# Kernel optimization log

Measured on AMD Instinct MI355X. Metric: run time of the kernel, lower is better.

Reference implementation:

```python
import jax, jax.numpy as jnp
from jax import lax
import numpy as np

NHEADS = 8

def _conv_block2d(x, w, b):
    y = lax.conv_general_dilated(x, w, (2, 2), [(1, 1), (1, 1)],
                                 dimension_numbers=('NCHW', 'OIHW', 'NCHW'))
    return jax.nn.gelu(y + b[None, :, None, None])

def _conv_block3d(x, w, b):
    y = lax.conv_general_dilated(x, w, (2, 2, 2), [(1, 1)] * 3,
                                 dimension_numbers=('NCDHW', 'OIDHW', 'NCDHW'))
    return jax.nn.gelu(y + b[None, :, None, None, None])

def _layernorm(x, g, b, eps=1e-5):
    mu = x.mean(-1, keepdims=True)
    var = x.var(-1, keepdims=True)
    return (x - mu) / jnp.sqrt(var + eps) * g + b

def _neighborhood_attn(x, g, bln, qkv_w, qkv_b, proj_w, proj_b, dw=5, hw=7, ww=7):
    # x: [B, C, D, H, W]; 3D neighborhood attention, window (dw,hw,ww), zero-pad + mask
    B, C, D, H, W = x.shape
    h, hd = NHEADS, C // NHEADS
    xt = jnp.transpose(x, (0, 2, 3, 4, 1))               # [B,D,H,W,C]
    y = _layernorm(xt, g, bln)
    qkv = y @ qkv_w + qkv_b                               # [B,D,H,W,3C]
    qkv = qkv.reshape(B, D, H, W, 3, h, hd)
    qkv = jnp.transpose(qkv, (4, 0, 5, 6, 1, 2, 3))       # [3,B,h,hd,D,H,W]
    q, k, v = qkv[0] * (hd ** -0.5), qkv[1], qkv[2]
    pz, py, px = dw // 2, hw // 2, ww // 2
    pad = ((0, 0), (0, 0), (0, 0), (pz, pz), (py, py), (px, px))
    kp, vp = jnp.pad(k, pad), jnp.pad(v, pad)
    valid = jnp.pad(jnp.ones((D, H, W), x.dtype), ((pz, pz), (py, py), (px, px)))
    offs = jnp.stack(jnp.meshgrid(jnp.arange(dw), jnp.arange(hw), jnp.arange(ww), indexing='ij'), -1).reshape(-1, 3)

    def score_step(_, o):
        ks = lax.dynamic_slice(kp, (0, 0, 0, o[0], o[1], o[2]), (B, h, hd, D, H, W))
        m = lax.dynamic_slice(valid, (o[0], o[1], o[2]), (D, H, W))
        return None, ((q * ks).sum(2), m)

    _, (scores, masks) = lax.scan(score_step, None, offs)  # [245,B,h,D,H,W],[245,D,H,W]
    neg = jnp.finfo(scores.dtype).min
    scores = jnp.where(masks[:, None, None] > 0, scores, neg)
    probs = jax.nn.softmax(scores, axis=0)

    def out_step(acc, xs):
        o, p = xs
        vs = lax.dynamic_slice(vp, (0, 0, 0, o[0], o[1], o[2]), (B, h, hd, D, H, W))
        return acc + p[:, :, None] * vs, None

    out0 = jnp.zeros((B, h, hd, D, H, W), x.dtype)
    out, _ = lax.scan(out_step, out0, (offs, probs))
    out = jnp.transpose(out, (0, 3, 4, 5, 1, 2)).reshape(B, D, H, W, C)
    out = out @ proj_w + proj_b
    return x + jnp.transpose(out, (0, 4, 1, 2, 3))

def setup_inputs() -> dict:
    key = jax.random.key(0)
    ks = jax.random.split(key, 16)
    rn = lambda i, shp, s: jax.random.normal(ks[i], shp, jnp.float32) * s
    return {
        'x_2d': rn(0, (1, 8, 256, 512), 1.0),
        'x_3d': rn(1, (1, 5, 24, 256, 512), 1.0),
        'sw0': rn(2, (128, 8, 3, 3), 0.02), 'sb0': jnp.zeros((128,), jnp.float32),
        'sw1': rn(3, (256, 128, 3, 3), 0.02), 'sb1': jnp.zeros((256,), jnp.float32),
        'sw2': rn(4, (512, 256, 3, 3), 0.02), 'sb2': jnp.zeros((512,), jnp.float32),
        'pw0': rn(5, (128, 5, 3, 3, 3), 0.02), 'pb0': jnp.zeros((128,), jnp.float32),
        'pw1': rn(6, (256, 128, 3, 3, 3), 0.02), 'pb1': jnp.zeros((256,), jnp.float32),
        'pw2': rn(7, (512, 256, 3, 3, 3), 0.02), 'pb2': jnp.zeros((512,), jnp.float32),
        'lat_w': rn(8, (512, 512, 1, 1, 1), 0.02), 'lat_b': jnp.zeros((512,), jnp.float32),
        'ln_g': jnp.ones((3, 512), jnp.float32), 'ln_b': jnp.zeros((3, 512), jnp.float32),
        'qkv_w': rn(9, (3, 512, 1536), 0.02), 'qkv_b': jnp.zeros((3, 1536), jnp.float32),
        'proj_w': rn(10, (3, 512, 512), 0.02), 'proj_b': jnp.zeros((3, 512), jnp.float32),
    }

def reference(x_2d, x_3d, sw0, sb0, sw1, sb1, sw2, sb2,
              pw0, pb0, pw1, pb1, pw2, pb2, lat_w, lat_b,
              ln_g, ln_b, qkv_w, qkv_b, proj_w, proj_b):
    s = x_2d
    for w_, b_ in ((sw0, sb0), (sw1, sb1), (sw2, sb2)):
        s = _conv_block2d(s, w_, b_)
    p = x_3d
    for w_, b_ in ((pw0, pb0), (pw1, pb1), (pw2, pb2)):
        p = _conv_block3d(p, w_, b_)
    feats = jnp.concatenate([p, s[:, :, None]], axis=2)   # [B,512,D/8+1,H/8,W/8]
    lat = lax.conv_general_dilated(feats, lat_w, (1, 1, 1), 'VALID',
                                   dimension_numbers=('NCDHW', 'OIDHW', 'NCDHW'))
    lat = lat + lat_b[None, :, None, None, None]
    for i in range(3):
        lat = _neighborhood_attn(lat, ln_g[i], ln_b[i], qkv_w[i], qkv_b[i], proj_w[i], proj_b[i])
    return lat
```

## Files before the change

### kernel.cpp

```cpp
#include <hip/hip_runtime.h>
#include <hip/hip_bf16.h>
#include <math.h>

typedef __hip_bfloat16 bf16;
typedef __attribute__((ext_vector_type(8))) short s8v;
typedef __attribute__((ext_vector_type(4))) float f4v;

__device__ __forceinline__ float ldf(const float* p) { return *p; }
__device__ __forceinline__ float ldf(const bf16* p) { return __bfloat162float(*p); }
__device__ __forceinline__ void stf(float* p, float v) { *p = v; }
__device__ __forceinline__ void stf(bf16* p, float v) { *p = __float2bfloat16(v); }

__device__ __forceinline__ float gelu_tanh(float x) {
    float x3 = x * x * x;
    return 0.5f * x * (1.f + tanhf(0.7978845608028654f * (x + 0.044715f * x3)));
}
__device__ __forceinline__ unsigned short bfbits(float x) {
    bf16 t = __float2bfloat16(x);
    return *(unsigned short*)&t;
}

__device__ __forceinline__ void gload16(const bf16* g, bf16* l)
{
    __builtin_amdgcn_global_load_lds(
        (const __attribute__((address_space(1))) unsigned int*)g,
        (__attribute__((address_space(3))) unsigned int*)l,
        16, 0, 0);
}

__global__ __launch_bounds__(256) void fill0_k(uint4* __restrict__ p, int n16)
{
    int i = blockIdx.x * 256 + threadIdx.x;
    if (i < n16) p[i] = uint4{0u, 0u, 0u, 0u};
}

__global__ __launch_bounds__(256) void wprep_k(const float* __restrict__ w, bf16* __restrict__ wr,
                                               int OC, int IC, int T)
{
    int i = blockIdx.x * 256 + threadIdx.x;
    if (i >= OC * IC * T) return;
    int t = i % T; int rem = i / T; int ic = rem % IC; int oc = rem / IC;
    wr[((size_t)t * OC + oc) * IC + ic] = __float2bfloat16(w[i]);
}

__global__ __launch_bounds__(256) void w1prep_k(const float* __restrict__ w, bf16* __restrict__ o,
                                                int OC, int nic, int ntap, int Kp)
{
    int i = blockIdx.x * 256 + threadIdx.x;
    if (i >= OC * Kp) return;
    int oc = i / Kp, k = i - oc * Kp;
    float v = 0.f;
    if (k < nic * ntap) {
        int tap = k / nic, ic = k - tap * nic;
        v = w[((size_t)oc * nic + ic) * ntap + tap];
    }
    o[i] = __float2bfloat16(v);
}

__global__ __launch_bounds__(256) void tprep_k(const float* __restrict__ w, bf16* __restrict__ wt,
                                               int K, int N)
{
    int i = blockIdx.x * 256 + threadIdx.x;
    if (i >= K * N) return;
    int n = i % N, k = i / N;
    wt[(size_t)n * K + k] = __float2bfloat16(w[i]);
}

__global__ __launch_bounds__(256) void cast_k(const float* __restrict__ w, bf16* __restrict__ o, int n)
{
    int i = blockIdx.x * 256 + threadIdx.x;
    if (i < n) o[i] = __float2bfloat16(w[i]);
}

__global__ __launch_bounds__(256) void im2col3d_k(const float* __restrict__ x, bf16* __restrict__ A, int od0)
{
    int gid = blockIdx.x * 256 + threadIdx.x;
    int m = gid / 20, kg = gid - 20 * (gid / 20);
    int ow = m & 255, rowid = m >> 8;
    int oh = rowid & 127, od = od0 + (rowid >> 7);
    int iz0 = 2 * od - 1, iy0 = 2 * oh - 1, ix0 = 2 * ow - 1;
    union { uint4 u; unsigned short h[8]; } pk;
#pragma unroll
    for (int j = 0; j < 8; j++) {
        int k = kg * 8 + j;
        float v = 0.f;
        if (k < 135) {
            int tap = k / 5, ic = k - tap * 5;
            int kz = tap / 9, r = tap - kz * 9;
            int ky = r / 3, kx = r - ky * 3;
            int iz = iz0 + kz, iy = iy0 + ky, ix = ix0 + kx;
            if ((unsigned)iz < 24u && (unsigned)iy < 256u && (unsigned)ix < 512u)
                v = x[(((size_t)ic * 24 + iz) * 256 + iy) * 512 + ix];
        }
        pk.h[j] = bfbits(v);
    }
    *(uint4*)&A[(size_t)m * 160 + kg * 8] = pk.u;
}

__global__ __launch_bounds__(256) void im2col2d_k(const float* __restrict__ x, bf16* __restrict__ A)
{
    int gid = blockIdx.x * 256 + threadIdx.x;
    int m = gid / 12, kg = gid - 12 * (gid / 12);
    int ow = m & 255, oh = m >> 8;
    int iy0 = 2 * oh - 1, ix0 = 2 * ow - 1;
    union { uint4 u; unsigned short h[8]; } pk;
#pragma unroll
    for (int j = 0; j < 8; j++) {
        int k = kg * 8 + j;
        float v = 0.f;
        if (k < 72) {
            int tap = k >> 3, ic = k & 7;
            int ky = tap / 3, kx = tap - ky * 3;
            int iy = iy0 + ky, ix = ix0 + kx;
            if ((unsigned)iy < 256u && (unsigned)ix < 512u)
                v = x[((size_t)ic * 256 + iy) * 512 + ix];
        }
        pk.h[j] = bfbits(v);
    }
    *(uint4*)&A[(size_t)m * 96 + kg * 8] = pk.u;
}

__global__ __launch_bounds__(256) void conv1_gemm(
    const bf16* __restrict__ A, const bf16* __restrict__ W, const float* __restrict__ bias,
    bf16* __restrict__ out, int M, int Kp, int rowOff)
{
    __shared__ __align__(16) bf16 As[128 * 32];
    __shared__ __align__(16) bf16 Bs[128 * 32];
    int tid = threadIdx.x;
    int m0 = blockIdx.x * 128;
    int wave = tid >> 6, lane = tid & 63;
    int wb = tid & 192;
    int wm = (wave >> 1) * 64, wn = (wave & 1) * 64;
    int lm = lane & 15, lq = lane >> 4;
    f4v acc[4][4];
#pragma unroll
    for (int i = 0; i < 4; i++)
#pragma unroll
        for (int j = 0; j < 4; j++) acc[i][j] = f4v{0.f, 0.f, 0.f, 0.f};
    for (int k0 = 0; k0 < Kp; k0 += 32) {
        __syncthreads();
#pragma unroll
        for (int c = 0; c < 2; c++) {
            int i = c * 256 + tid;
            int row = i >> 2, kq = i & 3;
            gload16(&A[(size_t)(m0 + row) * Kp + k0 + kq * 8], &As[(c * 256 + wb) * 8]);
            gload16(&W[(size_t)row * Kp + k0 + kq * 8], &Bs[(c * 256 + wb) * 8]);
        }
        __syncthreads();
        s8v af[4], bfr[4];
#pragma unroll
        for (int mi = 0; mi < 4; mi++) af[mi] = *(const s8v*)&As[(wm + mi * 16 + lm) * 32 + lq * 8];
#pragma unroll
        for (int ni = 0; ni < 4; ni++) bfr[ni] = *(const s8v*)&Bs[(wn + ni * 16 + lm) * 32 + lq * 8];
#pragma unroll
        for (int mi = 0; mi < 4; mi++)
#pragma unroll
            for (int ni = 0; ni < 4; ni++)
                acc[mi][ni] = __builtin_amdgcn_mfma_f32_16x16x32_bf16(af[mi], bfr[ni], acc[mi][ni], 0, 0, 0);
    }
#pragma unroll
    for (int mi = 0; mi < 4; mi++)
#pragma unroll
        for (int ni = 0; ni < 4; ni++)
#pragma unroll
            for (int r = 0; r < 4; r++) {
                int m = m0 + wm + mi * 16 + lq * 4 + r;
                int n = wn + ni * 16 + lm;
                int row = rowOff + (m >> 8), x = m & 255;
                float v = acc[mi][ni][r] + bias[n];
                out[((size_t)row * 258 + 1 + x) * 128 + n] = __float2bfloat16(gelu_tanh(v));
            }
}

template <int BM, int KD>
__global__ __launch_bounds__(256) void conv_mfma2(
    const bf16* __restrict__ in, const bf16* __restrict__ wr, const float* __restrict__ bias,
    bf16* __restrict__ out, int ID, int IH, int IWp, int IC,
    int OH, int OC, int OWS, int outPad, int nx)
{
    constexpr int NI = (BM == 128) ? 4 : 2;
    __shared__ __align__(16) bf16 As[3 * BM * 32];
    __shared__ __align__(16) bf16 Bs[3 * 128 * 32];
    int tid = threadIdx.x;
    int nwg = gridDim.x;
    int bl = blockIdx.x;
    int swz = (bl & 7) * (nwg >> 3) + (bl >> 3);
    int n0 = (swz % nx) * 128;
    int rowid = swz / nx;
    int od = rowid / OH, oh = rowid % OH;
    int wave = tid >> 6, lane = tid & 63;
    int wb = tid & 192;
    int wm = (BM == 128) ? (wave >> 1) * 64 : 0;
    int wn = (BM == 128) ? (wave & 1) * 64 : wave * 32;
    int lm = lane & 15, lq = lane >> 4;
    f4v acc[4][NI];
#pragma unroll
    for (int i = 0; i < 4; i++)
#pragma unroll
        for (int j = 0; j < NI; j++) acc[i][j] = f4v{0.f, 0.f, 0.f, 0.f};

    for (int kz = 0; kz < KD; kz++) {
        int iz = (KD == 3) ? (2 * od + kz - 1) : 0;
        if ((unsigned)iz >= (unsigned)ID) continue;
        for (int ky = 0; ky < 3; ky++) {
            int iy = 2 * oh + ky - 1;
            if ((unsigned)iy >= (unsigned)IH) continue;
            const bf16* inrow = in + ((size_t)iz * IH + iy) * IWp * IC;
            const bf16* wbase = wr + (size_t)((kz * 3 + ky) * 3) * OC * IC;
            for (int kb = 0; kb < IC; kb += 32) {
                __syncthreads();
#pragma unroll
                for (int c = 0; c < (3 * BM) / 64; c++) {
                    int i = c * 256 + tid;
                    int kx = i / (BM * 4);
                    int r = i - kx * (BM * 4);
                    int m = r >> 2, sub = r & 3;
                    gload16(&inrow[(size_t)(2 * m + kx) * IC + kb + sub * 8],
                            &As[(c * 256 + wb) * 8]);
                }
#pragma unroll
                for (int c = 0; c < 6; c++) {
                    int i = c * 256 + tid;
                    int t3 = i >> 9, r = i & 511, n = r >> 2, sub = r & 3;
                    gload16(&wbase[((size_t)t3 * OC + n0 + n) * IC + kb + sub * 8],
                            &Bs[(c * 256 + wb) * 8]);
                }
                __syncthreads();
#pragma unroll
                for (int kx = 0; kx < 3; kx++) {
                    s8v af[4], bfr[NI];
#pragma unroll
                    for (int mi = 0; mi < 4; mi++)
                        af[mi] = *(const s8v*)&As[(kx * BM + wm + mi * 16 + lm) * 32 + lq * 8];
#pragma unroll
                    for (int ni = 0; ni < NI; ni++)
                        bfr[ni] = *(const s8v*)&Bs[(kx * 128 + wn + ni * 16 + lm) * 32 + lq * 8];
#pragma unroll
                    for (int mi = 0; mi < 4; mi++)
#pragma unroll
                        for (int ni = 0; ni < NI; ni++)
                            acc[mi][ni] = __builtin_amdgcn_mfma_f32_16x16x32_bf16(af[mi], bfr[ni], acc[mi][ni], 0, 0, 0);
                }
            }
        }
    }
    size_t orowbase = ((size_t)rowid * OWS + outPad) * OC;
#pragma unroll
    for (int mi = 0; mi < 4; mi++)
#pragma unroll
        for (int ni = 0; ni < NI; ni++)
#pragma unroll
            for (int r = 0; r < 4; r++) {
                int m = wm + mi * 16 + lq * 4 + r;
                int n = n0 + wn + ni * 16 + lm;
                float v = acc[mi][ni][r] + bias[n];
                out[orowbase + (size_t)m * OC + n] = __float2bfloat16(gelu_tanh(v));
            }
}

template <typename OutT, int RES, int VT>
__global__ __launch_bounds__(256) void gemm_bt(
    const bf16* __restrict__ A, const bf16* __restrict__ Bt, const float* __restrict__ bias,
    OutT* __restrict__ C, const float* __restrict__ res, bf16* __restrict__ vt,
    int M, int N, int K)
{
    __shared__ __align__(16) bf16 As[128 * 32];
    __shared__ __align__(16) bf16 Bs[128 * 32];
    int tid = threadIdx.x;
    int n0 = blockIdx.x * 128, m0 = blockIdx.y * 128;
    int wave = tid >> 6, lane = tid & 63;
    int wb = tid & 192;
    int wm = (wave >> 1) * 64, wn = (wave & 1) * 64;
    int lm = lane & 15, lq = lane >> 4;
    f4v acc[4][4];
#pragma unroll
    for (int i = 0; i < 4; i++)
#pragma unroll
        for (int j = 0; j < 4; j++) acc[i][j] = f4v{0.f, 0.f, 0.f, 0.f};
    for (int k0 = 0; k0 < K; k0 += 32) {
        __syncthreads();
#pragma unroll
        for (int c = 0; c < 2; c++) {
            int i = c * 256 + tid;
            int row = i >> 2, kq = i & 3;
            gload16(&A[(size_t)(m0 + row) * K + k0 + kq * 8], &As[(c * 256 + wb) * 8]);
            gload16(&Bt[(size_t)(n0 + row) * K + k0 + kq * 8], &Bs[(c * 256 + wb) * 8]);
        }
        __syncthreads();
        s8v af[4], bfr[4];
#pragma unroll
        for (int mi = 0; mi < 4; mi++) af[mi] = *(const s8v*)&As[(wm + mi * 16 + lm) * 32 + lq * 8];
#pragma unroll
        for (int ni = 0; ni < 4; ni++) bfr[ni] = *(const s8v*)&Bs[(wn + ni * 16 + lm) * 32 + lq * 8];
#pragma unroll
        for (int mi = 0; mi < 4; mi++)
#pragma unroll
            for (int ni = 0; ni < 4; ni++)
                acc[mi][ni] = __builtin_amdgcn_mfma_f32_16x16x32_bf16(af[mi], bfr[ni], acc[mi][ni], 0, 0, 0);
    }
#pragma unroll
    for (int mi = 0; mi < 4; mi++)
#pragma unroll
        for (int ni = 0; ni < 4; ni++) {
            int n = n0 + wn + ni * 16 + lm;
            int mbase = m0 + wm + mi * 16 + lq * 4;
            float b = bias[n];
            if (VT && n >= 1024) {
                ushort4 pk;
                pk.x = bfbits(acc[mi][ni][0] + b);
                pk.y = bfbits(acc[mi][ni][1] + b);
                pk.z = bfbits(acc[mi][ni][2] + b);
                pk.w = bfbits(acc[mi][ni][3] + b);
                *(ushort4*)&vt[(size_t)(n - 1024) * 8192 + mbase] = pk;
            }
#pragma unroll
            for (int r = 0; r < 4; r++) {
                int m = mbase + r;
                float v = acc[mi][ni][r] + b;
                if (RES) v += res[(size_t)m * N + n];
                stf(&C[(size_t)m * N + n], v);
            }
        }
}

__global__ __launch_bounds__(256) void ln_k(
    const float* __restrict__ lat, const float* __restrict__ g, const float* __restrict__ b,
    bf16* __restrict__ y)
{
    int tok = blockIdx.x * 4 + (threadIdx.x >> 6);
    int lane = threadIdx.x & 63;
    const float4* row = (const float4*)&lat[(size_t)tok * 512 + lane * 8];
    float4 a = row[0], c = row[1];
    float s = a.x + a.y + a.z + a.w + c.x + c.y + c.z + c.w;
    float ss = a.x * a.x + a.y * a.y + a.z * a.z + a.w * a.w
             + c.x * c.x + c.y * c.y + c.z * c.z + c.w * c.w;
#pragma unroll
    for (int off = 32; off; off >>= 1) {
        s += __shfl_xor(s, off);
        ss += __shfl_xor(ss, off);
    }
    float mu = s * (1.f / 512.f);
    float var = ss * (1.f / 512.f) - mu * mu;
    float rstd = rsqrtf(var + 1e-5f);
    const float4* gp = (const float4*)&g[lane * 8];
    const float4* bp = (const float4*)&b[lane * 8];
    float4 g0 = gp[0], g1 = gp[1], b0 = bp[0], b1 = bp[1];
    union { uint4 u; unsigned short h[8]; } pk;
    pk.h[0] = bfbits((a.x - mu) * rstd * g0.x + b0.x);
    pk.h[1] = bfbits((a.y - mu) * rstd * g0.y + b0.y);
    pk.h[2] = bfbits((a.z - mu) * rstd * g0.z + b0.z);
    pk.h[3] = bfbits((a.w - mu) * rstd * g0.w + b0.w);
    pk.h[4] = bfbits((c.x - mu) * rstd * g1.x + b1.x);
    pk.h[5] = bfbits((c.y - mu) * rstd * g1.y + b1.y);
    pk.h[6] = bfbits((c.z - mu) * rstd * g1.z + b1.z);
    pk.h[7] = bfbits((c.w - mu) * rstd * g1.w + b1.w);
    *(uint4*)&y[(size_t)tok * 512 + lane * 8] = pk.u;
}

__global__ __launch_bounds__(512) void natt_mfma(
    const bf16* __restrict__ qkv, const bf16* __restrict__ vT, bf16* __restrict__ o)
{
    __shared__ __align__(16) char smem[40960];
    float* mlb = (float*)smem;
    float* obuf = (float*)(smem + 8192);
    int tid = threadIdx.x;
    int bx = blockIdx.x;
    int rd = bx >> 5, rh = bx & 31;
    int d = (rd == 0) ? 1 : (rd == 1) ? 2 : (rd == 2) ? 0 : 3;
    int h = (rh < 26) ? (rh + 3) : (rh == 26) ? 2 : (rh == 27) ? 29
          : (rh == 28) ? 1 : (rh == 29) ? 30 : (rh == 30) ? 0 : 31;
    int rowid = d * 32 + h;
    int head = blockIdx.y;
    int rowbase = rowid * 64;
    int hoff = head * 64;
    int wave = tid >> 6, lane = tid & 63;
    int olane = wave & 3, rhalf = wave >> 2;
    int lm = lane & 15, lq = lane >> 4;
    char* qsb = smem;
    bf16* pb = (bf16*)(smem + 8192 + olane * 8192);

    {
        int row = tid >> 3, sub = tid & 7;
        *(uint4*)(qsb + row * 128 + ((sub * 16) ^ ((row & 7) << 4))) =
            *(const uint4*)&qkv[(size_t)(rowbase + row) * 1536 + hoff + sub * 8];
    }
    {
        uint4 z{0u, 0u, 0u, 0u};
        uint4* zp = (uint4*)(smem + 8192);
        zp[tid] = z; zp[tid + 512] = z; zp[tid + 1024] = z; zp[tid + 1536] = z;
    }
    __syncthreads();

    f4v Oa[2][4];
#pragma unroll
    for (int i = 0; i < 2; i++)
#pragma unroll
        for (int j = 0; j < 4; j++) Oa[i][j] = f4v{0.f, 0.f, 0.f, 0.f};
    float mr[2][4], lr[2][4];
#pragma unroll
    for (int i = 0; i < 2; i++)
#pragma unroll
        for (int j = 0; j < 4; j++) { mr[i][j] = -1e30f; lr[i][j] = 0.f; }

    for (int idx = olane; idx < 35; idx += 4) {
        int dz = idx / 7 - 2, dy = idx % 7 - 3;
        int zz = d + dz, yy = h + dy;
        if ((unsigned)zz >= 4u || (unsigned)yy >= 32u) continue;
        int kbase = (zz * 32 + yy) * 64;
        s8v kf[4][2];
#pragma unroll
        for (int ni = 0; ni < 4; ni++)
#pragma unroll
            for (int c = 0; c < 2; c++)
                kf[ni][c] = *(const s8v*)&qkv[(size_t)(kbase + ni * 16 + lm) * 1536 + 512 + hoff + c * 32 + lq * 8];
#pragma unroll
        for (int mj = 0; mj < 2; mj++) {
            int mi = rhalf * 2 + mj;
            int qrow = mi * 16 + lm;
            s8v qc0 = *(const s8v*)(qsb + qrow * 128 + ((lq * 16) ^ ((qrow & 7) << 4)));
            s8v qc1 = *(const s8v*)(qsb + qrow * 128 + ((64 + lq * 16) ^ ((qrow & 7) << 4)));
            f4v s[4];
#pragma unroll
            for (int ni = 0; ni < 4; ni++) s[ni] = f4v{0.f, 0.f, 0.f, 0.f};
            __builtin_amdgcn_s_setprio(1);
#pragma unroll
            for (int ni = 0; ni < 4; ni++)
                s[ni] = __builtin_amdgcn_mfma_f32_16x16x32_bf16(qc0, kf[ni][0], s[ni], 0, 0, 0);
#pragma unroll
            for (int ni = 0; ni < 4; ni++)
                s[ni] = __builtin_amdgcn_mfma_f32_16x16x32_bf16(qc1, kf[ni][1], s[ni], 0, 0, 0);
            __builtin_amdgcn_s_setprio(0);
#pragma unroll
            for (int r = 0; r < 4; r++) {
                int w0 = mi * 16 + lq * 4 + r;
                float s0v = s[0][r], s1v = s[1][r], s2v = s[2][r], s3v = s[3][r];
                int t = w0 + 8 - lm;
                int niq = (t < 0) ? 0 : (t >> 4);
                niq = (niq > 3) ? 3 : niq;
                float vlo = (niq & 1) ? s1v : s0v;
                float vhi = (niq & 1) ? s3v : s2v;
                float v = (niq & 2) ? vhi : vlo;
                int col = (niq << 4) | lm;
                int dlt = col - w0;
                float vv = ((unsigned)(dlt + 3) <= 6u) ? v * 0.125f : -1e30f;
                float rm = vv;
#pragma unroll
                for (int off = 1; off <= 8; off <<= 1)
                    rm = fmaxf(rm, __shfl_xor(rm, off));
                float mo = mr[mj][r];
                float mn = mo;
                if (__any(rm > mo)) {
                    mn = fmaxf(mo, rm);
                    float al = __expf(mo - mn);
                    mr[mj][r] = mn;
                    lr[mj][r] *= al;
#pragma unroll
                    for (int nd = 0; nd < 4; nd++)
                        Oa[mj][nd][r] *= al;
                }
                float p = __expf(vv - mn);
                float rs = p;
#pragma unroll
                for (int off = 1; off <= 8; off <<= 1)
                    rs += __shfl_xor(rs, off);
                lr[mj][r] += rs;
                pb[(w0 << 6) + (col ^ ((w0 & 7) << 3))] = __float2bfloat16(p);
            }
        }
        s8v vf[4][2];
#pragma unroll
        for (int nd = 0; nd < 4; nd++)
#pragma unroll
            for (int c = 0; c < 2; c++)
                vf[nd][c] = *(const s8v*)&vT[(size_t)(hoff + nd * 16 + lm) * 8192 + kbase + c * 32 + lq * 8];
        __asm__ __volatile__("s_waitcnt lgkmcnt(0)" ::: "memory");
        __builtin_amdgcn_sched_barrier(0);
#pragma unroll
        for (int c = 0; c < 2; c++) {
            s8v pf[2];
#pragma unroll
            for (int mj = 0; mj < 2; mj++) {
                int mi = rhalf * 2 + mj;
                pf[mj] = *(const s8v*)&pb[((mi * 16 + lm) << 6) + ((c * 32 + lq * 8) ^ ((lm & 7) << 3))];
            }
            __builtin_amdgcn_s_setprio(1);
#pragma unroll
            for (int mj = 0; mj < 2; mj++)
#pragma unroll
                for (int nd = 0; nd < 4; nd++)
                    Oa[mj][nd] = __builtin_amdgcn_mfma_f32_16x16x32_bf16(pf[mj], vf[nd][c], Oa[mj][nd], 0, 0, 0);
            __builtin_amdgcn_s_setprio(0);
        }
    }
    __syncthreads();
    if (lm == 0) {
#pragma unroll
        for (int mj = 0; mj < 2; mj++)
#pragma unroll
            for (int r = 0; r < 4; r++) {
                int row = (rhalf * 2 + mj) * 16 + lq * 4 + r;
                mlb[olane * 128 + row] = mr[mj][r];
                mlb[olane * 128 + 64 + row] = lr[mj][r];
            }
    }
    __syncthreads();
    for (int wv = 0; wv < 4; wv++) {
        if (olane == wv) {
#pragma unroll
            for (int mj = 0; mj < 2; mj++)
#pragma unroll
                for (int r = 0; r < 4; r++) {
                    int row = (rhalf * 2 + mj) * 16 + lq * 4 + r;
                    float M = fmaxf(fmaxf(mlb[row], mlb[128 + row]),
                                    fmaxf(mlb[256 + row], mlb[384 + row]));
                    float sc = __expf(mr[mj][r] - M);
#pragma unroll
                    for (int nd = 0; nd < 4; nd++) {
                        int ci = row * 65 + nd * 16 + lm;
                        float add = Oa[mj][nd][r] * sc;
                        obuf[ci] = (wv == 0) ? add : (obuf[ci] + add);
                    }
                }
        }
        __syncthreads();
    }
    {
        int row = tid >> 3, cb = (tid & 7) * 8;
        float m0 = mlb[row], m1 = mlb[128 + row], m2 = mlb[256 + row], m3 = mlb[384 + row];
        float M = fmaxf(fmaxf(m0, m1), fmaxf(m2, m3));
        float L = mlb[64 + row] * __expf(m0 - M) + mlb[192 + row] * __expf(m1 - M)
                + mlb[320 + row] * __expf(m2 - M) + mlb[448 + row] * __expf(m3 - M);
        float inv = 1.f / L;
        union { uint4 u; unsigned short hs[8]; } pk;
#pragma unroll
        for (int j = 0; j < 8; j++)
            pk.hs[j] = bfbits(obuf[row * 65 + cb + j] * inv);
        *(uint4*)&o[(size_t)(rowbase + row) * 512 + hoff + cb] = pk.u;
    }
}

__global__ __launch_bounds__(256) void tout_k(const float* __restrict__ lat, float* __restrict__ out)
{
    __shared__ float t[64][65];
    int p0 = blockIdx.x * 64, c0 = blockIdx.y * 64;
    for (int i = threadIdx.x; i < 4096; i += 256) {
        int r = i >> 6, cc = i & 63;
        t[r][cc] = lat[(size_t)(p0 + r) * 512 + c0 + cc];
    }
    __syncthreads();
    for (int i = threadIdx.x; i < 4096; i += 256) {
        int cc = i >> 6, r = i & 63;
        out[(size_t)(c0 + cc) * 8192 + p0 + r] = t[r][cc];
    }
}

extern "C" void kernel_launch(void* const* d_in, const int* in_sizes, int n_in,
                              void* d_out, int out_size, void* d_ws, size_t ws_size,
                              hipStream_t stream)
{
    const float* x2d = (const float*)d_in[0];
    const float* x3d = (const float*)d_in[1];
    const float* sw0 = (const float*)d_in[2];
    const float* sb0 = (const float*)d_in[3];
    const float* sw1 = (const float*)d_in[4];
    const float* sb1 = (const float*)d_in[5];
    const float* sw2 = (const float*)d_in[6];
    const float* sb2 = (const float*)d_in[7];
    const float* pw0 = (const float*)d_in[8];
    const float* pb0 = (const float*)d_in[9];
    const float* pw1 = (const float*)d_in[10];
    const float* pb1 = (const float*)d_in[11];
    const float* pw2 = (const float*)d_in[12];
    const float* pb2 = (const float*)d_in[13];
    const float* latw = (const float*)d_in[14];
    const float* latb = (const float*)d_in[15];
    const float* lng = (const float*)d_in[16];
    const float* lnb = (const float*)d_in[17];
    const float* qkvw = (const float*)d_in[18];
    const float* qkvb = (const float*)d_in[19];
    const float* projw = (const float*)d_in[20];
    const float* projb = (const float*)d_in[21];
    float* outp = (float*)d_out;

    char* ws = (char*)d_ws;
    bf16* p0pad = (bf16*)(ws + 0);
    bf16* wr3d2 = (bf16*)(ws + 101449728ull);
    bf16* wr3d3 = (bf16*)(ws + 103219200ull);
    bf16* wr2d2 = (bf16*)(ws + 110297088ull);
    bf16* wr2d3 = (bf16*)(ws + 110886912ull);
    bf16* qkvt  = (bf16*)(ws + 113246208ull);
    bf16* projt = (bf16*)(ws + 117964800ull);
    bf16* latbf = (bf16*)(ws + 119537664ull);
    bf16* w13d  = (bf16*)(ws + 120061952ull);
    bf16* w12d  = (bf16*)(ws + 120102912ull);
    bf16* p1pad = (bf16*)(ws + 120127488ull);
    bf16* s0pad = (bf16*)(ws + 145686528ull);
    bf16* s1pad = (bf16*)(ws + 154140672ull);
    bf16* featsT= (bf16*)(ws + 158400512ull);
    float* lat  = (float*)(ws + 166789120ull);
    bf16* A3 = (bf16*)(ws + 120127488ull);
    bf16* A2 = (bf16*)(ws + 158400512ull);
    bf16* ybf    = (bf16*)(ws + 0);
    bf16* qkvbuf = (bf16*)(ws + 8388608ull);
    bf16* attno  = (bf16*)(ws + 33554432ull);
    bf16* vT     = (bf16*)(ws + 41943040ull);

    wprep_k<<<3456, 256, 0, stream>>>(pw1, wr3d2, 256, 128, 27);
    wprep_k<<<13824, 256, 0, stream>>>(pw2, wr3d3, 512, 256, 27);
    wprep_k<<<1152, 256, 0, stream>>>(sw1, wr2d2, 256, 128, 9);
    wprep_k<<<4608, 256, 0, stream>>>(sw2, wr2d3, 512, 256, 9);
    for (int r = 0; r < 3; r++) {
        tprep_k<<<3072, 256, 0, stream>>>(qkvw + (size_t)r * 786432, qkvt + (size_t)r * 786432, 512, 1536);
        tprep_k<<<1024, 256, 0, stream>>>(projw + (size_t)r * 262144, projt + (size_t)r * 262144, 512, 512);
    }
    cast_k<<<1024, 256, 0, stream>>>(latw, latbf, 262144);
    w1prep_k<<<80, 256, 0, stream>>>(pw0, w13d, 128, 5, 27, 160);
    w1prep_k<<<48, 256, 0, stream>>>(sw0, w12d, 128, 8, 9, 96);

    fill0_k<<<24768, 256, 0, stream>>>((uint4*)p0pad, 6340608);

    im2col3d_k<<<15360, 256, 0, stream>>>(x3d, A3, 0);
    conv1_gemm<<<1536, 256, 0, stream>>>(A3, w13d, pb0, p0pad, 196608, 160, 0);
    im2col3d_k<<<15360, 256, 0, stream>>>(x3d, A3, 6);
    conv1_gemm<<<1536, 256, 0, stream>>>(A3, w13d, pb0, p0pad, 196608, 160, 768);

    fill0_k<<<9344, 256, 0, stream>>>((uint4*)p1pad, 2392064);
    im2col2d_k<<<1536, 256, 0, stream>>>(x2d, A2);
    conv1_gemm<<<256, 256, 0, stream>>>(A2, w12d, sb0, s0pad, 32768, 96, 0);

    conv_mfma2<128, 1><<<dim3(128), 256, 0, stream>>>(s0pad, wr2d2, sb1, s1pad, 1, 128, 258, 128, 64, 256, 130, 1, 2);
    conv_mfma2<64, 1><<<dim3(128), 256, 0, stream>>>(s1pad, wr2d3, sb2, featsT + (size_t)6144 * 512, 1, 64, 130, 256, 32, 512, 64, 0, 4);
    conv_mfma2<128, 3><<<dim3(768), 256, 0, stream>>>(p0pad, wr3d2, pb1, p1pad, 12, 128, 258, 128, 64, 256, 130, 1, 2);
    conv_mfma2<64, 3><<<dim3(384), 256, 0, stream>>>(p1pad, wr3d3, pb2, featsT, 6, 64, 130, 256, 32, 512, 64, 0, 4);

    gemm_bt<float, 0, 0><<<dim3(4, 64), 256, 0, stream>>>(featsT, latbf, latb, lat, nullptr, nullptr, 8192, 512, 512);

    for (int r = 0; r < 3; r++) {
        ln_k<<<2048, 256, 0, stream>>>(lat, lng + r * 512, lnb + r * 512, ybf);
        gemm_bt<bf16, 0, 1><<<dim3(12, 64), 256, 0, stream>>>(ybf, qkvt + (size_t)r * 786432, qkvb + r * 1536,
                                                              qkvbuf, nullptr, vT, 8192, 1536, 512);
        natt_mfma<<<dim3(128, 8), 512, 0, stream>>>(qkvbuf, vT, attno);
        gemm_bt<float, 1, 0><<<dim3(4, 64), 256, 0, stream>>>(attno, projt + (size_t)r * 262144, projb + r * 512,
                                                              lat, lat, nullptr, 8192, 512, 512);
    }

    tout_k<<<dim3(128, 8), 256, 0, stream>>>(lat, outp);
}
```

Before: 1.213 ms.

## Zero only padding columns and transpose weights through shared-memory tiles

Replaces the full-buffer zero fills of the padded activation buffers with a kernel that zeroes only the left padding column of each row, which assumes the conv kernels write every other element, including the remaining padding. Weight prep kernels that did strided scattered writes are replaced by a shared-memory tiled transpose-and-cast kernel with coalesced reads and writes. This cuts prep memory traffic, but correctness now depends on the layout assumption that only the first column per row needs explicit zeroing; s0pad/s1pad are now also zeroed explicitly.

```diff
diff --git a/kernel.cpp b/kernel.cpp
--- a/kernel.cpp
+++ b/kernel.cpp
@@ -28,19 +28,31 @@
         16, 0, 0);
 }
 
-__global__ __launch_bounds__(256) void fill0_k(uint4* __restrict__ p, int n16)
+__global__ __launch_bounds__(256) void fillcol_k(uint4* __restrict__ p, int nrows,
+                                                 int strideGran, int granPerRow)
 {
     int i = blockIdx.x * 256 + threadIdx.x;
-    if (i < n16) p[i] = uint4{0u, 0u, 0u, 0u};
-}
-
-__global__ __launch_bounds__(256) void wprep_k(const float* __restrict__ w, bf16* __restrict__ wr,
-                                               int OC, int IC, int T)
-{
-    int i = blockIdx.x * 256 + threadIdx.x;
-    if (i >= OC * IC * T) return;
-    int t = i % T; int rem = i / T; int ic = rem % IC; int oc = rem / IC;
-    wr[((size_t)t * OC + oc) * IC + ic] = __float2bfloat16(w[i]);
+    int row = i / granPerRow, g = i - row * granPerRow;
+    if (row < nrows) p[(size_t)row * strideGran + g] = uint4{0u, 0u, 0u, 0u};
+}
+
+__global__ __launch_bounds__(256) void tcast_k(const float* __restrict__ in,
+                                               bf16* __restrict__ out, int R, int C)
+{
+    __shared__ float t[64][65];
+    int r0 = blockIdx.x * 64, c0 = blockIdx.y * 64;
+    for (int i = threadIdx.x; i < 4096; i += 256) {
+        int rr = i >> 6, cc = i & 63;
+        int r = r0 + rr, c = c0 + cc;
+        t[rr][cc] = (c < C) ? in[(size_t)r * C + c] : 0.f;
+    }
+    __syncthreads();
+    for (int i = threadIdx.x; i < 4096; i += 256) {
+        int cc = i >> 6, rr = i & 63;
+        int r = r0 + rr, c = c0 + cc;
+        if (c < C)
+            out[(size_t)c * R + r] = __float2bfloat16(t[rr][cc]);
+    }
 }
 
 __global__ __launch_bounds__(256) void w1prep_k(const float* __restrict__ w, bf16* __restrict__ o,
@@ -55,15 +67,6 @@
         v = w[((size_t)oc * nic + ic) * ntap + tap];
     }
     o[i] = __float2bfloat16(v);
-}
-
-__global__ __launch_bounds__(256) void tprep_k(const float* __restrict__ w, bf16* __restrict__ wt,
-                                               int K, int N)
-{
-    int i = blockIdx.x * 256 + threadIdx.x;
-    if (i >= K * N) return;
-    int n = i % N, k = i / N;
-    wt[(size_t)n * K + k] = __float2bfloat16(w[i]);
 }
 
 __global__ __launch_bounds__(256) void cast_k(const float* __restrict__ w, bf16* __restrict__ o, int n)
@@ -605,26 +608,28 @@
     bf16* attno  = (bf16*)(ws + 33554432ull);
     bf16* vT     = (bf16*)(ws + 41943040ull);
 
-    wprep_k<<<3456, 256, 0, stream>>>(pw1, wr3d2, 256, 128, 27);
-    wprep_k<<<13824, 256, 0, stream>>>(pw2, wr3d3, 512, 256, 27);
-    wprep_k<<<1152, 256, 0, stream>>>(sw1, wr2d2, 256, 128, 9);
-    wprep_k<<<4608, 256, 0, stream>>>(sw2, wr2d3, 512, 256, 9);
+    tcast_k<<<dim3(512, 1), 256, 0, stream>>>(pw1, wr3d2, 32768, 27);
+    tcast_k<<<dim3(2048, 1), 256, 0, stream>>>(pw2, wr3d3, 131072, 27);
+    tcast_k<<<dim3(512, 1), 256, 0, stream>>>(sw1, wr2d2, 32768, 9);
+    tcast_k<<<dim3(2048, 1), 256, 0, stream>>>(sw2, wr2d3, 131072, 9);
     for (int r = 0; r < 3; r++) {
-        tprep_k<<<3072, 256, 0, stream>>>(qkvw + (size_t)r * 786432, qkvt + (size_t)r * 786432, 512, 1536);
-        tprep_k<<<1024, 256, 0, stream>>>(projw + (size_t)r * 262144, projt + (size_t)r * 262144, 512, 512);
+        tcast_k<<<dim3(8, 24), 256, 0, stream>>>(qkvw + (size_t)r * 786432, qkvt + (size_t)r * 786432, 512, 1536);
+        tcast_k<<<dim3(8, 8), 256, 0, stream>>>(projw + (size_t)r * 262144, projt + (size_t)r * 262144, 512, 512);
     }
     cast_k<<<1024, 256, 0, stream>>>(latw, latbf, 262144);
     w1prep_k<<<80, 256, 0, stream>>>(pw0, w13d, 128, 5, 27, 160);
     w1prep_k<<<48, 256, 0, stream>>>(sw0, w12d, 128, 8, 9, 96);
 
-    fill0_k<<<24768, 256, 0, stream>>>((uint4*)p0pad, 6340608);
+    fillcol_k<<<96, 256, 0, stream>>>((uint4*)p0pad, 1536, 4128, 16);
 
     im2col3d_k<<<15360, 256, 0, stream>>>(x3d, A3, 0);
     conv1_gemm<<<1536, 256, 0, stream>>>(A3, w13d, pb0, p0pad, 196608, 160, 0);
     im2col3d_k<<<15360, 256, 0, stream>>>(x3d, A3, 6);
     conv1_gemm<<<1536, 256, 0, stream>>>(A3, w13d, pb0, p0pad, 196608, 160, 768);
 
-    fill0_k<<<9344, 256, 0, stream>>>((uint4*)p1pad, 2392064);
+    fillcol_k<<<48, 256, 0, stream>>>((uint4*)p1pad, 384, 4160, 32);
+    fillcol_k<<<8, 256, 0, stream>>>((uint4*)s0pad, 128, 4128, 16);
+    fillcol_k<<<8, 256, 0, stream>>>((uint4*)s1pad, 64, 4160, 32);
     im2col2d_k<<<1536, 256, 0, stream>>>(x2d, A2);
     conv1_gemm<<<256, 256, 0, stream>>>(A2, w12d, sb0, s0pad, 32768, 96, 0);
 
```

Result: no change. 1.234 ms (+1.7%).
